# Kernel optimization log

Hardware: AMD Instinct MI355X
Metric: run time of the kernel (lower is better)

The kernel has to match this reference:

```python
import jax, jax.numpy as jnp
import numpy as np

# dims per module source / chosen globals
B, LB = 4, 28            # new frames, buffered frames; M = B+LB = L = 32
DK, DV = 256, 32         # Dk=256 hardcoded; Dv = 4*len_of_lookup+4 with len_of_lookup=7
HS, WS = 64, 64          # H//8, W//8 with H=W=512
LMAX = 32                # memory cap L
TRAIN_SZ = 1000          # log base train_sz
ALPHA = 0.5              # blend coefficient (original inits 0, which zeroes the branch)
# log(L*h*w + h*w, train_sz) / sqrt(Dk)
SCALE = float(np.log(LMAX * HS * WS + HS * WS) / np.log(TRAIN_SZ) / np.sqrt(DK))


def _xavier(key, fan_in, fan_out):
    lim = np.sqrt(6.0 / (fan_in + fan_out))
    return jax.random.uniform(key, (fan_in, fan_out), jnp.float32, -lim, lim)


def setup_inputs() -> dict:
    key = jax.random.key(0)
    ks = jax.random.split(key, 7)
    return {
        "fc": jax.random.normal(ks[0], (B, DK, HS, WS), jnp.float32),
        "fm": jax.random.normal(ks[1], (B, DV, HS, WS), jnp.float32),
        "key_buffer": jax.random.normal(ks[2], (LB, DK, HS, WS), jnp.float32),
        "value_buffer": jax.random.normal(ks[3], (LB, DV, HS, WS), jnp.float32),
        "Q": _xavier(ks[4], DK, DK),
        "K": _xavier(ks[5], DK, DK),
        "V": _xavier(ks[6], DV, DV),
    }


def reference(fc, fm, key_buffer, value_buffer, Q, K, V):
    # matmul = einsum('ijkl,jm->imkl'): per-pixel channel mixing
    q = jnp.einsum('bdhw,de->behw', fc, Q)                      # [B,Dk,h,w]
    k = jnp.concatenate([jnp.einsum('bdhw,de->behw', fc, K), key_buffer], axis=0)    # [M,Dk,h,w]
    v = jnp.concatenate([jnp.einsum('bdhw,de->behw', fm, V), value_buffer], axis=0)  # [M,Dv,h,w]
    # current_batch (=1) < L, so no slicing of k/v on this step
    scores = SCALE * jnp.einsum('bdhw,mdhw->bmhw', q, k)        # [B,M,h,w]
    attn = jax.nn.softmax(scores, axis=-1)                      # NOTE: softmax over width axis, as in source (dim=-1)
    ctx = jnp.einsum('bmhw,mdhw->bdhw', attn, v)                # [B,Dv,h,w]
    return fm + ALPHA * ctx
```

## Files before the change

### kernel.cpp

```cpp
#include <hip/hip_runtime.h>
#include <hip/hip_bf16.h>
#include <cmath>

#define NB 4
#define NM 32
#define DKc 256
#define DVc 32
#define NP 4096

using bf16x8 = __attribute__((ext_vector_type(8))) short;
using f32x4  = __attribute__((ext_vector_type(4))) float;

__device__ __forceinline__ unsigned short f2bf(float f) {
    union { float f; unsigned u; } x; x.f = f;
    unsigned r = 0x7FFFu + ((x.u >> 16) & 1u);
    return (unsigned short)((x.u + r) >> 16);
}
__device__ __forceinline__ float bflo(unsigned u) { union { unsigned u; float f; } x; x.u = u << 16; return x.f; }
__device__ __forceinline__ float bfhi(unsigned u) { union { unsigned u; float f; } x; x.u = u & 0xffff0000u; return x.f; }
__device__ __forceinline__ float bf2f(unsigned short s) { union { unsigned u; float f; } x; x.u = ((unsigned)s) << 16; return x.f; }

__global__ __launch_bounds__(256) void k_transpose_bf16(
    const float* __restrict__ src, unsigned short* __restrict__ dst,
    int R, int C, long batchStride) {
    __shared__ float tile[64][65];
    int b = blockIdx.z;
    const float* s = src + (long)b * batchStride;
    unsigned short* d = dst + (long)b * batchStride;
    int r0 = blockIdx.y * 64, c0 = blockIdx.x * 64;
    int t = threadIdx.x;
    #pragma unroll
    for (int j = 0; j < 16; ++j) {
        int i = t + 256 * j;
        int r = i >> 6, c = i & 63;
        tile[r][c] = s[(long)(r0 + r) * C + c0 + c];
    }
    __syncthreads();
    #pragma unroll
    for (int j = 0; j < 8; ++j) {
        int i = t + 256 * j;
        int row = i >> 5;
        int pr = i & 31;
        float f0 = tile[2 * pr][row];
        float f1 = tile[2 * pr + 1][row];
        unsigned pack = (unsigned)f2bf(f0) | ((unsigned)f2bf(f1) << 16);
        reinterpret_cast<unsigned*>(d)[(((long)(c0 + row) * R + r0) >> 1) + pr] = pack;
    }
}

__global__ __launch_bounds__(256) void k_vproj(
    const float* __restrict__ fm, const float* __restrict__ V, float* __restrict__ vproj) {
    __shared__ float Vl[32][32];
    __shared__ float fml[32][256];
    int b = blockIdx.y, p0 = blockIdx.x * 256, t = threadIdx.x;
    #pragma unroll
    for (int j = 0; j < 4; ++j) { int i = t + 256 * j; Vl[i >> 5][i & 31] = V[i]; }
    for (int j = 0; j < 32; ++j) {
        int i = t + 256 * j;
        int dd = i >> 8, c = i & 255;
        fml[dd][c] = fm[((long)b * DVc + dd) * NP + p0 + c];
    }
    __syncthreads();
    float acc[32];
    #pragma unroll
    for (int e = 0; e < 32; ++e) acc[e] = 0.f;
    for (int dd = 0; dd < 32; ++dd) {
        float fv = fml[dd][t];
        #pragma unroll
        for (int e = 0; e < 32; ++e) acc[e] += fv * Vl[dd][e];
    }
    #pragma unroll
    for (int e = 0; e < 32; ++e) vproj[((long)b * DVc + e) * NP + p0 + t] = acc[e];
}

__global__ __launch_bounds__(256) void k_proj_gemm(
    const unsigned short* __restrict__ WTq, const unsigned short* __restrict__ WTk,
    const unsigned short* __restrict__ fcT,
    unsigned short* __restrict__ qT, float* __restrict__ kproj) {
    int t = threadIdx.x;
    int wave = t >> 6, lane = t & 63;
    int b = blockIdx.z & 3, mat = blockIdx.z >> 2;
    int e0 = blockIdx.y * 64 + wave * 16;
    int p0 = blockIdx.x * 64;
    int ln = lane & 15, quad = lane >> 4;
    const unsigned short* WT = mat ? WTk : WTq;
    const unsigned short* aptr = WT + (long)(e0 + ln) * DKc + quad * 8;
    const unsigned short* bbase = fcT + ((long)b * NP + p0 + ln) * DKc + quad * 8;
    f32x4 acc[4] = {};
    for (int kk = 0; kk < DKc; kk += 32) {
        bf16x8 a = *reinterpret_cast<const bf16x8*>(aptr + kk);
        #pragma unroll
        for (int j = 0; j < 4; ++j) {
            bf16x8 bb = *reinterpret_cast<const bf16x8*>(bbase + (long)j * 16 * DKc + kk);
            acc[j] = __builtin_amdgcn_mfma_f32_16x16x32_bf16(a, bb, acc[j], 0, 0, 0);
        }
    }
    int eb = e0 + quad * 4;
    if (mat == 0) {
        #pragma unroll
        for (int j = 0; j < 4; ++j)
            #pragma unroll
            for (int r = 0; r < 4; ++r) {
                int e = eb + r, p = p0 + j * 16 + ln;
                qT[((long)b * NP + p) * DKc + e] = f2bf(acc[j][r]);
            }
    } else {
        #pragma unroll
        for (int j = 0; j < 4; ++j)
            #pragma unroll
            for (int r = 0; r < 4; ++r) {
                int e = eb + r, p = p0 + j * 16 + ln;
                kproj[((long)b * DKc + e) * NP + p] = acc[j][r];
            }
    }
}

__global__ __launch_bounds__(512) void k_scores(
    const unsigned short* __restrict__ qT, const float* __restrict__ kproj,
    const float* __restrict__ kbuf, float* __restrict__ scores, float scale) {
    __shared__ float red[16][4][4][32];
    int t = threadIdx.x;
    int g = t >> 5, p = t & 31;
    int p0 = blockIdx.x * 32;
    int mg = blockIdx.y;
    float qreg[4][16];
    #pragma unroll
    for (int b = 0; b < 4; ++b) {
        const uint4* qp4 = reinterpret_cast<const uint4*>(qT + ((long)b * NP + p0 + p) * DKc + g * 16);
        uint4 u0 = qp4[0], u1 = qp4[1];
        unsigned w[8] = {u0.x, u0.y, u0.z, u0.w, u1.x, u1.y, u1.z, u1.w};
        #pragma unroll
        for (int j = 0; j < 8; ++j) { qreg[b][2 * j] = bflo(w[j]); qreg[b][2 * j + 1] = bfhi(w[j]); }
    }
    for (int c = 0; c < 4; ++c) {
        float acc[4][4];
        #pragma unroll
        for (int mi = 0; mi < 4; ++mi)
            #pragma unroll
            for (int b = 0; b < 4; ++b) acc[mi][b] = 0.f;
        #pragma unroll
        for (int mi = 0; mi < 4; ++mi) {
            int m = mg * 16 + c * 4 + mi;
            const float* kp = (m < 4 ? kproj + (long)m * DKc * NP : kbuf + (long)(m - 4) * DKc * NP)
                              + (long)(g * 16) * NP + p0 + p;
            #pragma unroll
            for (int j = 0; j < 16; ++j) {
                float kv = kp[(long)j * NP];
                acc[mi][0] += qreg[0][j] * kv;
                acc[mi][1] += qreg[1][j] * kv;
                acc[mi][2] += qreg[2][j] * kv;
                acc[mi][3] += qreg[3][j] * kv;
            }
        }
        #pragma unroll
        for (int mi = 0; mi < 4; ++mi)
            #pragma unroll
            for (int b = 0; b < 4; ++b) red[g][mi][b][p] = acc[mi][b];
        __syncthreads();
        {
            int mi = t >> 7, b = (t >> 5) & 3, pp = t & 31;
            float s = 0.f;
            #pragma unroll
            for (int gg = 0; gg < 16; ++gg) s += red[gg][mi][b][pp];
            int m = mg * 16 + c * 4 + mi;
            scores[((long)b * NM + m) * NP + p0 + pp] = scale * s;
        }
        __syncthreads();
    }
}

__global__ __launch_bounds__(256) void k_out(
    const float* __restrict__ scores, const float* __restrict__ vproj,
    const float* __restrict__ vbuf, const float* __restrict__ fm,
    float* __restrict__ out) {
    __shared__ unsigned short attn[128][130];
    int t = threadIdx.x;
    int p0 = blockIdx.x * 128;
    int dq = blockIdx.y;
    {
        int b = t >> 6, mrow = (t >> 1) & 31, hs = t & 1;
        const f32x4* s4 = reinterpret_cast<const f32x4*>(scores + ((long)b * NM + mrow) * NP + p0 + hs * 64);
        f32x4 v[16];
        #pragma unroll
        for (int j = 0; j < 16; ++j) v[j] = s4[j];
        float mx = v[0][0];
        #pragma unroll
        for (int j = 0; j < 16; ++j)
            #pragma unroll
            for (int k = 0; k < 4; ++k) mx = fmaxf(mx, v[j][k]);
        float sum = 0.f;
        #pragma unroll
        for (int j = 0; j < 16; ++j)
            #pragma unroll
            for (int k = 0; k < 4; ++k) { float e = __expf(v[j][k] - mx); v[j][k] = e; sum += e; }
        float inv = 1.f / sum;
        unsigned short* arow = &attn[(b << 5) | mrow][hs * 64];
        #pragma unroll
        for (int j = 0; j < 16; ++j)
            #pragma unroll
            for (int k = 0; k < 4; ++k) arow[j * 4 + k] = f2bf(v[j][k] * inv);
    }
    __syncthreads();
    int p = t & 127, grp = t >> 7;
    int b0 = grp * 2, b1 = grp * 2 + 1;
    float acc0[8], acc1[8];
    #pragma unroll
    for (int d = 0; d < 8; ++d) { acc0[d] = 0.f; acc1[d] = 0.f; }
    for (int m = 0; m < 32; ++m) {
        float a0 = bf2f(attn[b0 * 32 + m][p]);
        float a1 = bf2f(attn[b1 * 32 + m][p]);
        const float* vbp = (m < 4 ? vproj + (long)m * DVc * NP : vbuf + (long)(m - 4) * DVc * NP)
                           + (long)(dq * 8) * NP + p0 + p;
        #pragma unroll
        for (int d = 0; d < 8; ++d) {
            float vv = vbp[(long)d * NP];
            acc0[d] += a0 * vv;
            acc1[d] += a1 * vv;
        }
    }
    #pragma unroll
    for (int d = 0; d < 8; ++d) {
        long i0 = ((long)b0 * DVc + dq * 8 + d) * NP + p0 + p;
        out[i0] = fm[i0] + 0.5f * acc0[d];
        long i1 = ((long)b1 * DVc + dq * 8 + d) * NP + p0 + p;
        out[i1] = fm[i1] + 0.5f * acc1[d];
    }
}

extern "C" void kernel_launch(void* const* d_in, const int* in_sizes, int n_in,
                              void* d_out, int out_size, void* d_ws, size_t ws_size,
                              hipStream_t stream) {
    const float* fc = (const float*)d_in[0];
    const float* fm = (const float*)d_in[1];
    const float* kb = (const float*)d_in[2];
    const float* vb = (const float*)d_in[3];
    const float* Q  = (const float*)d_in[4];
    const float* K  = (const float*)d_in[5];
    const float* V  = (const float*)d_in[6];
    float* out = (float*)d_out;
    char* ws = (char*)d_ws;
    unsigned short* fcT   = (unsigned short*)(ws);
    unsigned short* WTq   = (unsigned short*)(ws + 8388608);
    unsigned short* WTk   = (unsigned short*)(ws + 8519680);
    unsigned short* qT    = (unsigned short*)(ws + 8650752);
    float*          kproj = (float*)(ws + 17039360);
    float*          vproj = (float*)(ws + 33816576);
    float*          scores= (float*)(ws + 35913728);
    float scale = (float)(log(135168.0) / log(1000.0) / 16.0);

    hipLaunchKernelGGL(k_transpose_bf16, dim3(64, 4, 4), dim3(256), 0, stream,
                       fc, fcT, 256, 4096, (long)256 * 4096);
    hipLaunchKernelGGL(k_transpose_bf16, dim3(4, 4, 1), dim3(256), 0, stream,
                       Q, WTq, 256, 256, (long)0);
    hipLaunchKernelGGL(k_transpose_bf16, dim3(4, 4, 1), dim3(256), 0, stream,
                       K, WTk, 256, 256, (long)0);
    hipLaunchKernelGGL(k_vproj, dim3(16, 4), dim3(256), 0, stream, fm, V, vproj);
    hipLaunchKernelGGL(k_proj_gemm, dim3(64, 4, 8), dim3(256), 0, stream,
                       WTq, WTk, fcT, qT, kproj);
    hipLaunchKernelGGL(k_scores, dim3(128, 2), dim3(512), 0, stream,
                       qT, kproj, kb, scores, scale);
    hipLaunchKernelGGL(k_out, dim3(32, 4), dim3(256), 0, stream,
                       scores, vproj, vb, fm, out);
}
```

Baseline: 267.5 us.

## Split score and output kernels finer, fuse weight transposes, use nontemporal loads

k_scores now covers 8 memory slots per block instead of 16, which doubles its grid, and gets a min-blocks launch bound. k_out now covers 64 pixels per block instead of 128, with each width row's softmax split across two lanes and combined by xor shuffles; this also doubles its grid. The two weight transposes become a single launch, and the streaming key and value reads use nontemporal loads. The aim is to put more blocks in flight on the bandwidth-bound stages and save a launch, at the cost of reloading q registers in more blocks and a tighter register budget.

```diff
diff --git a/kernel.cpp b/kernel.cpp
--- a/kernel.cpp
+++ b/kernel.cpp
@@ -45,6 +45,33 @@
         float f1 = tile[2 * pr + 1][row];
         unsigned pack = (unsigned)f2bf(f0) | ((unsigned)f2bf(f1) << 16);
         reinterpret_cast<unsigned*>(d)[(((long)(c0 + row) * R + r0) >> 1) + pr] = pack;
+    }
+}
+
+__global__ __launch_bounds__(256) void k_transpose_w2(
+    const float* __restrict__ srcQ, unsigned short* __restrict__ dstQ,
+    const float* __restrict__ srcK, unsigned short* __restrict__ dstK) {
+    __shared__ float tile[64][65];
+    const float* s = blockIdx.z ? srcK : srcQ;
+    unsigned short* d = blockIdx.z ? dstK : dstQ;
+    int r0 = blockIdx.y * 64, c0 = blockIdx.x * 64;
+    int t = threadIdx.x;
+    #pragma unroll
+    for (int j = 0; j < 16; ++j) {
+        int i = t + 256 * j;
+        int r = i >> 6, c = i & 63;
+        tile[r][c] = s[(long)(r0 + r) * 256 + c0 + c];
+    }
+    __syncthreads();
+    #pragma unroll
+    for (int j = 0; j < 8; ++j) {
+        int i = t + 256 * j;
+        int row = i >> 5;
+        int pr = i & 31;
+        float f0 = tile[2 * pr][row];
+        float f1 = tile[2 * pr + 1][row];
+        unsigned pack = (unsigned)f2bf(f0) | ((unsigned)f2bf(f1) << 16);
+        reinterpret_cast<unsigned*>(d)[(((long)(c0 + row) * 256 + r0) >> 1) + pr] = pack;
     }
 }
 
@@ -115,7 +142,7 @@
     }
 }
 
-__global__ __launch_bounds__(512) void k_scores(
+__global__ __launch_bounds__(512, 4) void k_scores(
     const unsigned short* __restrict__ qT, const float* __restrict__ kproj,
     const float* __restrict__ kbuf, float* __restrict__ scores, float scale) {
     __shared__ float red[16][4][4][32];
@@ -132,7 +159,7 @@
         #pragma unroll
         for (int j = 0; j < 8; ++j) { qreg[b][2 * j] = bflo(w[j]); qreg[b][2 * j + 1] = bfhi(w[j]); }
     }
-    for (int c = 0; c < 4; ++c) {
+    for (int c = 0; c < 2; ++c) {
         float acc[4][4];
         #pragma unroll
         for (int mi = 0; mi < 4; ++mi)
@@ -140,12 +167,12 @@
             for (int b = 0; b < 4; ++b) acc[mi][b] = 0.f;
         #pragma unroll
         for (int mi = 0; mi < 4; ++mi) {
-            int m = mg * 16 + c * 4 + mi;
+            int m = mg * 8 + c * 4 + mi;
             const float* kp = (m < 4 ? kproj + (long)m * DKc * NP : kbuf + (long)(m - 4) * DKc * NP)
                               + (long)(g * 16) * NP + p0 + p;
             #pragma unroll
             for (int j = 0; j < 16; ++j) {
-                float kv = kp[(long)j * NP];
+                float kv = __builtin_nontemporal_load(kp + (long)j * NP);
                 acc[mi][0] += qreg[0][j] * kv;
                 acc[mi][1] += qreg[1][j] * kv;
                 acc[mi][2] += qreg[2][j] * kv;
@@ -162,7 +189,7 @@
             float s = 0.f;
             #pragma unroll
             for (int gg = 0; gg < 16; ++gg) s += red[gg][mi][b][pp];
-            int m = mg * 16 + c * 4 + mi;
+            int m = mg * 8 + c * 4 + mi;
             scores[((long)b * NM + m) * NP + p0 + pp] = scale * s;
         }
         __syncthreads();
@@ -173,57 +200,58 @@
     const float* __restrict__ scores, const float* __restrict__ vproj,
     const float* __restrict__ vbuf, const float* __restrict__ fm,
     float* __restrict__ out) {
-    __shared__ unsigned short attn[128][130];
-    int t = threadIdx.x;
-    int p0 = blockIdx.x * 128;
+    __shared__ unsigned short attn[128][66];
+    int t = threadIdx.x;
+    int p0 = blockIdx.x * 64;
     int dq = blockIdx.y;
     {
-        int b = t >> 6, mrow = (t >> 1) & 31, hs = t & 1;
-        const f32x4* s4 = reinterpret_cast<const f32x4*>(scores + ((long)b * NM + mrow) * NP + p0 + hs * 64);
-        f32x4 v[16];
-        #pragma unroll
-        for (int j = 0; j < 16; ++j) v[j] = s4[j];
+        int row = t >> 1;
+        int b = row >> 5, m = row & 31;
+        int hs = t & 1;
+        const f32x4* s4 = reinterpret_cast<const f32x4*>(scores + ((long)b * NM + m) * NP + p0 + hs * 32);
+        f32x4 v[8];
+        #pragma unroll
+        for (int j = 0; j < 8; ++j) v[j] = s4[j];
         float mx = v[0][0];
         #pragma unroll
-        for (int j = 0; j < 16; ++j)
+        for (int j = 0; j < 8; ++j)
             #pragma unroll
             for (int k = 0; k < 4; ++k) mx = fmaxf(mx, v[j][k]);
+        mx = fmaxf(mx, __shfl_xor(mx, 1));
         float sum = 0.f;
         #pragma unroll
-        for (int j = 0; j < 16; ++j)
+        for (int j = 0; j < 8; ++j)
             #pragma unroll
             for (int k = 0; k < 4; ++k) { float e = __expf(v[j][k] - mx); v[j][k] = e; sum += e; }
+        sum += __shfl_xor(sum, 1);
         float inv = 1.f / sum;
-        unsigned short* arow = &attn[(b << 5) | mrow][hs * 64];
-        #pragma unroll
-        for (int j = 0; j < 16; ++j)
+        unsigned short* arow = &attn[row][hs * 32];
+        #pragma unroll
+        for (int j = 0; j < 8; ++j)
             #pragma unroll
             for (int k = 0; k < 4; ++k) arow[j * 4 + k] = f2bf(v[j][k] * inv);
     }
     __syncthreads();
-    int p = t & 127, grp = t >> 7;
-    int b0 = grp * 2, b1 = grp * 2 + 1;
-    float acc0[8], acc1[8];
-    #pragma unroll
-    for (int d = 0; d < 8; ++d) { acc0[d] = 0.f; acc1[d] = 0.f; }
-    for (int m = 0; m < 32; ++m) {
-        float a0 = bf2f(attn[b0 * 32 + m][p]);
-        float a1 = bf2f(attn[b1 * 32 + m][p]);
-        const float* vbp = (m < 4 ? vproj + (long)m * DVc * NP : vbuf + (long)(m - 4) * DVc * NP)
-                           + (long)(dq * 8) * NP + p0 + p;
+    {
+        int px = t & 63, b = t >> 6;
+        float acc[8];
+        #pragma unroll
+        for (int d = 0; d < 8; ++d) acc[d] = 0.f;
+        for (int m = 0; m < 32; ++m) {
+            float a = bf2f(attn[b * 32 + m][px]);
+            const float* vbp = (m < 4 ? vproj + (long)m * DVc * NP : vbuf + (long)(m - 4) * DVc * NP)
+                               + (long)(dq * 8) * NP + p0 + px;
+            #pragma unroll
+            for (int d = 0; d < 8; ++d) {
+                float vv = __builtin_nontemporal_load(vbp + (long)d * NP);
+                acc[d] += a * vv;
+            }
+        }
         #pragma unroll
         for (int d = 0; d < 8; ++d) {
-            float vv = vbp[(long)d * NP];
-            acc0[d] += a0 * vv;
-            acc1[d] += a1 * vv;
-        }
-    }
-    #pragma unroll
-    for (int d = 0; d < 8; ++d) {
-        long i0 = ((long)b0 * DVc + dq * 8 + d) * NP + p0 + p;
-        out[i0] = fm[i0] + 0.5f * acc0[d];
-        long i1 = ((long)b1 * DVc + dq * 8 + d) * NP + p0 + p;
-        out[i1] = fm[i1] + 0.5f * acc1[d];
+            long i = ((long)b * DVc + dq * 8 + d) * NP + p0 + px;
+            out[i] = fm[i] + 0.5f * acc[d];
+        }
     }
 }
 
@@ -250,15 +278,13 @@
 
     hipLaunchKernelGGL(k_transpose_bf16, dim3(64, 4, 4), dim3(256), 0, stream,
                        fc, fcT, 256, 4096, (long)256 * 4096);
-    hipLaunchKernelGGL(k_transpose_bf16, dim3(4, 4, 1), dim3(256), 0, stream,
-                       Q, WTq, 256, 256, (long)0);
-    hipLaunchKernelGGL(k_transpose_bf16, dim3(4, 4, 1), dim3(256), 0, stream,
-                       K, WTk, 256, 256, (long)0);
+    hipLaunchKernelGGL(k_transpose_w2, dim3(4, 4, 2), dim3(256), 0, stream,
+                       Q, WTq, K, WTk);
     hipLaunchKernelGGL(k_vproj, dim3(16, 4), dim3(256), 0, stream, fm, V, vproj);
     hipLaunchKernelGGL(k_proj_gemm, dim3(64, 4, 8), dim3(256), 0, stream,
                        WTq, WTk, fcT, qT, kproj);
-    hipLaunchKernelGGL(k_scores, dim3(128, 2), dim3(512), 0, stream,
+    hipLaunchKernelGGL(k_scores, dim3(128, 4), dim3(512), 0, stream,
                        qT, kproj, kb, scores, scale);
-    hipLaunchKernelGGL(k_out, dim3(32, 4), dim3(256), 0, stream,
+    hipLaunchKernelGGL(k_out, dim3(64, 4), dim3(256), 0, stream,
                        scores, vproj, vb, fm, out);
 }
```

Result: slower. 283.6 us (+6.0%).
